# Kernel tuning notes

Hardware: AMD Instinct MI355X
Metric: run time of the kernel (lower is better)

The kernel has to match this reference:

```python
import jax, jax.numpy as jnp
import numpy as np

H = 16  # head_num

def _rope(x, cos, sin):
    # x: [B,H,T,dh]; cos/sin: [T, dh//2]
    xr = x.reshape(*x.shape[:-1], -1, 2)
    re, im = xr[..., 0], xr[..., 1]
    out_re = re * cos - im * sin
    out_im = re * sin + im * cos
    return jnp.stack([out_re, out_im], axis=-1).reshape(x.shape)

def setup_inputs() -> dict:
    key = jax.random.key(0)
    ks = jax.random.split(key, 5)
    B, T, D = 2, 2048, 1024
    s = 1.0 / np.sqrt(D)
    return {
        "embedding_word": jax.random.normal(ks[0], (B, T, D), jnp.float32),
        "wq": jax.random.normal(ks[1], (D, D), jnp.float32) * s,
        "wk": jax.random.normal(ks[2], (D, D), jnp.float32) * s,
        "wv": jax.random.normal(ks[3], (D, D), jnp.float32) * s,
        "wo": jax.random.normal(ks[4], (D, D), jnp.float32) * s,
    }

def reference(embedding_word, wq, wk, wv, wo):
    x = embedding_word
    B, T, D = x.shape
    dh = D // H
    # projections (torch Linear: x @ W.T)
    q = (x @ wq.T).reshape(B, T, H, dh).transpose(0, 2, 1, 3)  # [B,H,T,dh]
    k = (x @ wk.T).reshape(B, T, H, dh).transpose(0, 2, 1, 3)
    v = (x @ wv.T).reshape(B, T, H, dh).transpose(0, 2, 1, 3)
    # rotary embedding (theta=10000)
    freqs = 1.0 / (10000.0 ** (jnp.arange(0, dh, 2, dtype=jnp.float32) / dh))
    ang = jnp.arange(T, dtype=jnp.float32)[:, None] * freqs[None, :]  # [T, dh/2]
    cos, sin = jnp.cos(ang), jnp.sin(ang)
    q = _rope(q, cos, sin)
    k = _rope(k, cos, sin)
    # attention with causal mask; scale after mask as in original
    scores = jnp.einsum("bhqd,bhkd->bhqk", q, k)
    causal = jnp.triu(jnp.ones((T, T), dtype=bool), k=1)
    scores = jnp.where(causal, -jnp.inf, scores)
    weights = jax.nn.softmax(scores / jnp.sqrt(jnp.float32(dh)), axis=-1)
    out = jnp.einsum("bhqk,bhkd->bhqd", weights, v)
    out = out.transpose(0, 2, 1, 3).reshape(B, T, D)
    return out @ wo.T
```

## Files before the change

kernel.cpp:

```cpp
#include <hip/hip_runtime.h>
#include <hip/hip_bf16.h>
#include <math.h>

#define B_  2
#define T_  2048
#define D_  1024
#define H_  16
#define DH_ 64
#define TOK (B_*T_)

typedef __attribute__((ext_vector_type(8))) short bf16x8;
typedef __attribute__((ext_vector_type(4))) float f32x4;

static __device__ __forceinline__ float bf2f(short u) {
    union { unsigned int i; float f; } c;
    c.i = ((unsigned int)(unsigned short)u) << 16;
    return c.f;
}
static __device__ __forceinline__ short f2bf(float f) {
    union { float f; unsigned int i; } c; c.f = f;
    unsigned int r = c.i + 0x7fff + ((c.i >> 16) & 1);
    return (short)(r >> 16);
}

__global__ __launch_bounds__(256) void cast_bf16(const float* __restrict__ in,
                                                 short* __restrict__ out, int n8)
{
    int i = blockIdx.x * 256 + threadIdx.x;
    if (i < n8) {
        const float4* p = reinterpret_cast<const float4*>(in);
        float4 a = p[2*i], b = p[2*i+1];
        bf16x8 o;
        o[0] = f2bf(a.x); o[1] = f2bf(a.y); o[2] = f2bf(a.z); o[3] = f2bf(a.w);
        o[4] = f2bf(b.x); o[5] = f2bf(b.y); o[6] = f2bf(b.z); o[7] = f2bf(b.w);
        reinterpret_cast<bf16x8*>(out)[i] = o;
    }
}

__global__ __launch_bounds__(256) void rope_table(float2* __restrict__ tab)
{
    int idx = blockIdx.x * 256 + threadIdx.x;
    int t = idx >> 5, i = idx & 31;
    float freq = __powf(10000.f, -(float)i * (1.0f / 32.0f));
    float s, c;
    sincosf((float)t * freq, &s, &c);
    tab[idx] = make_float2(c, s);
}

__global__ __launch_bounds__(256) void rope_apply(short* __restrict__ X,
                                                  const float2* __restrict__ tab)
{
    int q = blockIdx.x * 256 + threadIdx.x;
    int p0 = q << 2;
    int tt = (p0 >> 9) & (T_ - 1);
    int i0 = p0 & 31;
    int4 v = reinterpret_cast<int4*>(X)[q];
    int out[4]; int vv[4] = {v.x, v.y, v.z, v.w};
#pragma unroll
    for (int j = 0; j < 4; ++j) {
        float2 cs = tab[tt * 32 + i0 + j];
        float re = bf2f((short)(vv[j] & 0xffff));
        float im = bf2f((short)(((unsigned int)vv[j]) >> 16));
        float nr = re * cs.x - im * cs.y;
        float ni = re * cs.y + im * cs.x;
        out[j] = (int)(unsigned short)f2bf(nr) |
                 ((int)(unsigned short)f2bf(ni) << 16);
    }
    reinterpret_cast<int4*>(X)[q] = make_int4(out[0], out[1], out[2], out[3]);
}

template<int BF16OUT>
__global__ __launch_bounds__(256) void gemm_abt_mfma(
    const short* __restrict__ A,
    const short* __restrict__ B0, const short* __restrict__ B1, const short* __restrict__ B2,
    short* __restrict__ Ob0, short* __restrict__ Ob1, short* __restrict__ Ob2,
    float* __restrict__ Of0, int K)
{
    __shared__ short As[128 * 32];
    __shared__ short Bs[128 * 32];
    const int sel = blockIdx.x >> 3;
    const int bn  = (blockIdx.x & 7) << 7;
    const int bm  = blockIdx.y << 7;
    const short* Bm = sel == 0 ? B0 : (sel == 1 ? B1 : B2);
    short* Obp      = sel == 0 ? Ob0 : (sel == 1 ? Ob1 : Ob2);
    const int tid  = threadIdx.x;
    const int wv   = tid >> 6, lane = tid & 63;
    const int wr   = wv >> 1,  wc   = wv & 1;
    const int fr   = lane & 15, fg  = lane >> 4;
    const int srow  = lane >> 2;
    const int skoff = (lane & 3) << 3;
    f32x4 acc[4][4] = {};

    for (int k0 = 0; k0 < K; k0 += 32) {
        __syncthreads();
#pragma unroll
        for (int it = 0; it < 2; ++it) {
            const int c = wv * 2 + it;
            const int r = 16 * c + srow;
            __builtin_amdgcn_global_load_lds(
                (const __attribute__((address_space(1))) unsigned int*)
                    (A + (size_t)(bm + r) * K + k0 + skoff),
                (__attribute__((address_space(3))) unsigned int*)(As + c * 512),
                16, 0, 0);
            __builtin_amdgcn_global_load_lds(
                (const __attribute__((address_space(1))) unsigned int*)
                    (Bm + (size_t)(bn + r) * K + k0 + skoff),
                (__attribute__((address_space(3))) unsigned int*)(Bs + c * 512),
                16, 0, 0);
        }
        __syncthreads();
        bf16x8 af[4], bfr[4];
#pragma unroll
        for (int m = 0; m < 4; ++m)
            af[m] = *(const bf16x8*)(As + (wr * 64 + m * 16 + fr) * 32 + fg * 8);
#pragma unroll
        for (int n = 0; n < 4; ++n)
            bfr[n] = *(const bf16x8*)(Bs + (wc * 64 + n * 16 + fr) * 32 + fg * 8);
#pragma unroll
        for (int m = 0; m < 4; ++m)
#pragma unroll
            for (int n = 0; n < 4; ++n)
                acc[m][n] = __builtin_amdgcn_mfma_f32_16x16x32_bf16(
                                af[m], bfr[n], acc[m][n], 0, 0, 0);
    }
    const int row0 = bm + wr * 64 + fg * 4;
    const int col0 = bn + wc * 64 + fr;
#pragma unroll
    for (int m = 0; m < 4; ++m)
#pragma unroll
        for (int n = 0; n < 4; ++n)
#pragma unroll
            for (int j = 0; j < 4; ++j) {
                const size_t idx = (size_t)(row0 + m * 16 + j) * 1024 + col0 + n * 16;
                if (BF16OUT) Obp[idx] = f2bf(acc[m][n][j]);
                else         Of0[idx] = acc[m][n][j];
            }
}

__global__ __launch_bounds__(256) void attn_mfma(
    const short* __restrict__ Qb, const short* __restrict__ Kb,
    const short* __restrict__ Vb, short* __restrict__ Ob)
{
    __shared__ short Ks[64 * 64];
    __shared__ short Vt[64 * 64];
    __shared__ short Ps[64 * 64];

    const int qt = (int)(gridDim.x - 1) - (int)blockIdx.x;
    const int bh = blockIdx.y;
    const int b  = bh >> 4, h = bh & 15;
    const int q0 = qt << 6;
    const int tid  = threadIdx.x;
    const int wv   = tid >> 6, lane = tid & 63;
    const int fr   = lane & 15, fg = lane >> 4;

    const size_t qrow = (size_t)(b * T_ + q0 + wv * 16 + fr);
    const short* qp = Qb + qrow * D_ + h * DH_;
    const bf16x8 qf0 = *(const bf16x8*)(qp + fg * 8);
    const bf16x8 qf1 = *(const bf16x8*)(qp + 32 + fg * 8);

    float m_i[4], l_i[4];
    f32x4 oa[4] = {};
#pragma unroll
    for (int j = 0; j < 4; ++j) { m_i[j] = -1e30f; l_i[j] = 0.f; }

    const int sdoff = (tid & 7) << 3;
    const int sr0   = tid >> 3;
    const int sr1   = sr0 + 32;
    const short* kbase = Kb + (size_t)b * T_ * D_ + h * DH_ + sdoff;
    const short* vbase = Vb + (size_t)b * T_ * D_ + h * DH_ + sdoff;

    for (int kt = 0; kt <= qt; ++kt) {
        const int k0 = kt << 6;
        const bf16x8 kr0 = *(const bf16x8*)(kbase + (size_t)(k0 + sr0) * D_);
        const bf16x8 kr1 = *(const bf16x8*)(kbase + (size_t)(k0 + sr1) * D_);
        const bf16x8 vr0 = *(const bf16x8*)(vbase + (size_t)(k0 + sr0) * D_);
        const bf16x8 vr1 = *(const bf16x8*)(vbase + (size_t)(k0 + sr1) * D_);
        __syncthreads();
        *(bf16x8*)(Ks + ((sr0 * 64 + sdoff) ^ ((sr0 & 7) << 3))) = kr0;
        *(bf16x8*)(Ks + ((sr1 * 64 + sdoff) ^ ((sr1 & 7) << 3))) = kr1;
#pragma unroll
        for (int jj = 0; jj < 8; ++jj) {
            const int j0 = (jj + (tid & 7)) & 7;
            const int d0 = sdoff + j0;
            Vt[(d0 * 64 + sr0) ^ ((d0 & 7) << 3)] = vr0[j0];
            Vt[(d0 * 64 + sr1) ^ ((d0 & 7) << 3)] = vr1[j0];
        }
        __syncthreads();

        f32x4 sc[4] = {};
#pragma unroll
        for (int f = 0; f < 4; ++f) {
            const int krow = 16 * f + fr;
            const bf16x8 b0 = *(const bf16x8*)(Ks + ((krow * 64 + fg * 8)      ^ ((krow & 7) << 3)));
            const bf16x8 b1 = *(const bf16x8*)(Ks + ((krow * 64 + 32 + fg * 8) ^ ((krow & 7) << 3)));
            sc[f] = __builtin_amdgcn_mfma_f32_16x16x32_bf16(qf0, b0, sc[f], 0, 0, 0);
            sc[f] = __builtin_amdgcn_mfma_f32_16x16x32_bf16(qf1, b1, sc[f], 0, 0, 0);
        }

#pragma unroll
        for (int j = 0; j < 4; ++j) {
            const int qg = q0 + 16 * wv + 4 * fg + j;
            float pv[4];
#pragma unroll
            for (int f = 0; f < 4; ++f) {
                const int kg = k0 + 16 * f + fr;
                const float x = sc[f][j] * 0.125f;
                pv[f] = (kg <= qg) ? x : -1e30f;
            }
            float mv = fmaxf(fmaxf(pv[0], pv[1]), fmaxf(pv[2], pv[3]));
            mv = fmaxf(mv, __shfl_xor(mv, 1));
            mv = fmaxf(mv, __shfl_xor(mv, 2));
            mv = fmaxf(mv, __shfl_xor(mv, 4));
            mv = fmaxf(mv, __shfl_xor(mv, 8));
            const float mnew = fmaxf(m_i[j], mv);
            const float corr = __expf(m_i[j] - mnew);
            m_i[j] = mnew;
            float ps = 0.f;
            const int qa = 16 * wv + 4 * fg + j;
#pragma unroll
            for (int f = 0; f < 4; ++f) {
                const float e = __expf(pv[f] - mnew);
                ps += e;
                Ps[(qa * 64 + 16 * f + fr) ^ ((qa & 7) << 3)] = f2bf(e);
            }
            ps += __shfl_xor(ps, 1); ps += __shfl_xor(ps, 2);
            ps += __shfl_xor(ps, 4); ps += __shfl_xor(ps, 8);
            l_i[j] = l_i[j] * corr + ps;
#pragma unroll
            for (int n = 0; n < 4; ++n) oa[n][j] *= corr;
        }

#pragma unroll
        for (int kc = 0; kc < 2; ++kc) {
            const int qa = 16 * wv + fr;
            const bf16x8 pa = *(const bf16x8*)(Ps + ((qa * 64 + kc * 32 + fg * 8) ^ ((qa & 7) << 3)));
#pragma unroll
            for (int n = 0; n < 4; ++n) {
                const int dr = 16 * n + fr;
                const bf16x8 vb = *(const bf16x8*)(Vt + ((dr * 64 + kc * 32 + fg * 8) ^ ((dr & 7) << 3)));
                oa[n] = __builtin_amdgcn_mfma_f32_16x16x32_bf16(pa, vb, oa[n], 0, 0, 0);
            }
        }
    }

#pragma unroll
    for (int j = 0; j < 4; ++j) {
        const float inv = 1.f / l_i[j];
        const size_t orow = (size_t)(b * T_ + q0 + 16 * wv + 4 * fg + j);
#pragma unroll
        for (int n = 0; n < 4; ++n)
            Ob[orow * D_ + h * DH_ + 16 * n + fr] = f2bf(oa[n][j] * inv);
    }
}

extern "C" void kernel_launch(void* const* d_in, const int* in_sizes, int n_in,
                              void* d_out, int out_size, void* d_ws, size_t ws_size,
                              hipStream_t stream)
{
    const float* x  = (const float*)d_in[0];
    const float* wq = (const float*)d_in[1];
    const float* wk = (const float*)d_in[2];
    const float* wv = (const float*)d_in[3];
    const float* wo = (const float*)d_in[4];
    float* out = (float*)d_out;

    const size_t NTOK = (size_t)TOK * D_;
    const size_t NW   = (size_t)D_ * D_;
    short* xb  = (short*)d_ws;
    short* wqb = xb  + NTOK;
    short* wkb = wqb + NW;
    short* wvb = wkb + NW;
    short* wob = wvb + NW;
    short* Qb  = wob + NW;
    short* Kb  = Qb  + NTOK;
    short* Vb  = Kb  + NTOK;
    short* Obf = Vb  + NTOK;
    float2* tab = (float2*)(Obf + NTOK);

    cast_bf16<<<2048, 256, 0, stream>>>(x,  xb,  (int)(NTOK / 8));
    cast_bf16<<<512,  256, 0, stream>>>(wq, wqb, (int)(NW / 8));
    cast_bf16<<<512,  256, 0, stream>>>(wk, wkb, (int)(NW / 8));
    cast_bf16<<<512,  256, 0, stream>>>(wv, wvb, (int)(NW / 8));
    cast_bf16<<<512,  256, 0, stream>>>(wo, wob, (int)(NW / 8));
    rope_table<<<256, 256, 0, stream>>>(tab);

    gemm_abt_mfma<1><<<dim3(24, 32), 256, 0, stream>>>(
        xb, wqb, wkb, wvb, Qb, Kb, Vb, nullptr, D_);

    rope_apply<<<2048, 256, 0, stream>>>(Qb, tab);
    rope_apply<<<2048, 256, 0, stream>>>(Kb, tab);

    attn_mfma<<<dim3(T_ / 64, B_ * H_), 256, 0, stream>>>(Qb, Kb, Vb, Obf);

    gemm_abt_mfma<0><<<dim3(8, 32), 256, 0, stream>>>(
        Obf, wob, wob, wob, nullptr, nullptr, nullptr, out, D_);
}
```

Before: 318.1 us.

## Rewrite attention with 32x32 MFMA, register-resident P, double buffering; fuse cast/rope launches

The attention kernel is rewritten so each block handles 128 query rows. It uses 32x32x16 MFMA, keeps the probability tile in registers through lane shuffles instead of shared memory, double-buffers the K/V tiles, and skips the rescale when the running max barely moves. The softmax scale and log2(e) are folded into Q during RoPE, so the kernel can use exp2f. The cast and rope kernels are merged into single launches, and the output is staged through shared memory for coalesced stores. These changes aim to cut LDS traffic, barriers, exp cost and launch overhead, at the price of more registers and bf16 rounding of the pre-scaled Q.

```diff
diff --git a/kernel.cpp b/kernel.cpp
--- a/kernel.cpp
+++ b/kernel.cpp
@@ -9,8 +9,9 @@
 #define DH_ 64
 #define TOK (B_*T_)
 
-typedef __attribute__((ext_vector_type(8))) short bf16x8;
-typedef __attribute__((ext_vector_type(4))) float f32x4;
+typedef __attribute__((ext_vector_type(8)))  short bf16x8;
+typedef __attribute__((ext_vector_type(4)))  float f32x4;
+typedef __attribute__((ext_vector_type(16))) float f32x16;
 
 static __device__ __forceinline__ float bf2f(short u) {
     union { unsigned int i; float f; } c;
@@ -22,19 +23,35 @@
     unsigned int r = c.i + 0x7fff + ((c.i >> 16) & 1);
     return (short)(r >> 16);
 }
-
-__global__ __launch_bounds__(256) void cast_bf16(const float* __restrict__ in,
-                                                 short* __restrict__ out, int n8)
+static __device__ __forceinline__ unsigned cvtpk(float lo, float hi2) {
+    unsigned r;
+    asm("v_cvt_pk_bf16_f32 %0, %1, %2" : "=v"(r) : "v"(lo), "v"(hi2));
+    return r;
+}
+
+__global__ __launch_bounds__(256) void cast_all(
+    const float* __restrict__ x,  const float* __restrict__ wq,
+    const float* __restrict__ wk, const float* __restrict__ wv,
+    const float* __restrict__ wo,
+    short* __restrict__ xb,  short* __restrict__ wqb,
+    short* __restrict__ wkb, short* __restrict__ wvb,
+    short* __restrict__ wob)
 {
     int i = blockIdx.x * 256 + threadIdx.x;
-    if (i < n8) {
-        const float4* p = reinterpret_cast<const float4*>(in);
-        float4 a = p[2*i], b = p[2*i+1];
-        bf16x8 o;
-        o[0] = f2bf(a.x); o[1] = f2bf(a.y); o[2] = f2bf(a.z); o[3] = f2bf(a.w);
-        o[4] = f2bf(b.x); o[5] = f2bf(b.y); o[6] = f2bf(b.z); o[7] = f2bf(b.w);
-        reinterpret_cast<bf16x8*>(out)[i] = o;
-    }
+    const float* src; short* dst; int off;
+    if (i < 524288) { src = x; dst = xb; off = i; }
+    else {
+        int j = i - 524288;
+        int wsel = j >> 17;  off = j & 131071;
+        src = wsel == 0 ? wq : wsel == 1 ? wk : wsel == 2 ? wv : wo;
+        dst = wsel == 0 ? wqb : wsel == 1 ? wkb : wsel == 2 ? wvb : wob;
+    }
+    const float4* p = reinterpret_cast<const float4*>(src);
+    float4 a = p[2*off], b = p[2*off+1];
+    bf16x8 o;
+    o[0] = f2bf(a.x); o[1] = f2bf(a.y); o[2] = f2bf(a.z); o[3] = f2bf(a.w);
+    o[4] = f2bf(b.x); o[5] = f2bf(b.y); o[6] = f2bf(b.z); o[7] = f2bf(b.w);
+    reinterpret_cast<bf16x8*>(dst)[off] = o;
 }
 
 __global__ __launch_bounds__(256) void rope_table(float2* __restrict__ tab)
@@ -47,10 +64,16 @@
     tab[idx] = make_float2(c, s);
 }
 
-__global__ __launch_bounds__(256) void rope_apply(short* __restrict__ X,
-                                                  const float2* __restrict__ tab)
-{
-    int q = blockIdx.x * 256 + threadIdx.x;
+__global__ __launch_bounds__(256) void rope_apply2(short* __restrict__ Q,
+                                                   short* __restrict__ K,
+                                                   const float2* __restrict__ tab)
+{
+    int g = blockIdx.x * 256 + threadIdx.x;
+    short* X;
+    float sc;
+    int q;
+    if (g < 524288) { X = Q; sc = 0.18033688011112042f; q = g; }
+    else            { X = K; sc = 1.0f;                 q = g - 524288; }
     int p0 = q << 2;
     int tt = (p0 >> 9) & (T_ - 1);
     int i0 = p0 & 31;
@@ -61,8 +84,8 @@
         float2 cs = tab[tt * 32 + i0 + j];
         float re = bf2f((short)(vv[j] & 0xffff));
         float im = bf2f((short)(((unsigned int)vv[j]) >> 16));
-        float nr = re * cs.x - im * cs.y;
-        float ni = re * cs.y + im * cs.x;
+        float nr = (re * cs.x - im * cs.y) * sc;
+        float ni = (re * cs.y + im * cs.x) * sc;
         out[j] = (int)(unsigned short)f2bf(nr) |
                  ((int)(unsigned short)f2bf(ni) << 16);
     }
@@ -137,120 +160,167 @@
             }
 }
 
-__global__ __launch_bounds__(256) void attn_mfma(
+__global__ __launch_bounds__(256) void attn_mfma2(
     const short* __restrict__ Qb, const short* __restrict__ Kb,
     const short* __restrict__ Vb, short* __restrict__ Ob)
 {
-    __shared__ short Ks[64 * 64];
-    __shared__ short Vt[64 * 64];
-    __shared__ short Ps[64 * 64];
-
-    const int qt = (int)(gridDim.x - 1) - (int)blockIdx.x;
+    __shared__ short KsBuf[2][64 * 64];
+    __shared__ short VtBuf[2][64 * 64];
+
+    const int qb = (int)(gridDim.x - 1 - blockIdx.x);
     const int bh = blockIdx.y;
     const int b  = bh >> 4, h = bh & 15;
-    const int q0 = qt << 6;
+    const int q0 = qb << 7;
     const int tid  = threadIdx.x;
-    const int wv   = tid >> 6, lane = tid & 63;
-    const int fr   = lane & 15, fg = lane >> 4;
-
-    const size_t qrow = (size_t)(b * T_ + q0 + wv * 16 + fr);
-    const short* qp = Qb + qrow * D_ + h * DH_;
-    const bf16x8 qf0 = *(const bf16x8*)(qp + fg * 8);
-    const bf16x8 qf1 = *(const bf16x8*)(qp + 32 + fg * 8);
-
-    float m_i[4], l_i[4];
-    f32x4 oa[4] = {};
-#pragma unroll
-    for (int j = 0; j < 4; ++j) { m_i[j] = -1e30f; l_i[j] = 0.f; }
-
-    const int sdoff = (tid & 7) << 3;
-    const int sr0   = tid >> 3;
-    const int sr1   = sr0 + 32;
-    const short* kbase = Kb + (size_t)b * T_ * D_ + h * DH_ + sdoff;
-    const short* vbase = Vb + (size_t)b * T_ * D_ + h * DH_ + sdoff;
-
-    for (int kt = 0; kt <= qt; ++kt) {
-        const int k0 = kt << 6;
-        const bf16x8 kr0 = *(const bf16x8*)(kbase + (size_t)(k0 + sr0) * D_);
-        const bf16x8 kr1 = *(const bf16x8*)(kbase + (size_t)(k0 + sr1) * D_);
-        const bf16x8 vr0 = *(const bf16x8*)(vbase + (size_t)(k0 + sr0) * D_);
-        const bf16x8 vr1 = *(const bf16x8*)(vbase + (size_t)(k0 + sr1) * D_);
+    const int w    = tid >> 6, lane = tid & 63;
+    const int ql   = lane & 31, hi = lane >> 5;
+    const int qw_lo  = q0 + 32 * w;
+    const int q_glob = qw_lo + ql;
+    const int nt = (q0 + 128) >> 6;
+
+    const short* qp = Qb + (size_t)(b * T_ + q_glob) * D_ + h * DH_ + hi * 8;
+    bf16x8 qf[4];
+#pragma unroll
+    for (int ds = 0; ds < 4; ++ds)
+        qf[ds] = *(const bf16x8*)(qp + 16 * ds);
+
+    float m_run = -3e38f, l_run = 0.f;
+    f32x16 accO0, accO1;
+#pragma unroll
+    for (int r = 0; r < 16; ++r) { accO0[r] = 0.f; accO1[r] = 0.f; }
+
+    const int sr0 = tid >> 3, sr1 = sr0 + 32, sdo = (tid & 7) << 3;
+    const short* kbase = Kb + (size_t)b * T_ * D_ + h * DH_ + sdo;
+    const short* vbase = Vb + (size_t)b * T_ * D_ + h * DH_ + sdo;
+
+    bf16x8 krA, krB, vrA, vrB;
+#define LOADT(t) {                                                        \
+        const size_t o_ = (size_t)((t) << 6) * D_;                        \
+        krA = *(const bf16x8*)(kbase + o_ + (size_t)sr0 * D_);            \
+        krB = *(const bf16x8*)(kbase + o_ + (size_t)sr1 * D_);            \
+        vrA = *(const bf16x8*)(vbase + o_ + (size_t)sr0 * D_);            \
+        vrB = *(const bf16x8*)(vbase + o_ + (size_t)sr1 * D_); }
+#define STORET(bu) {                                                      \
+        short* Kp = KsBuf[bu]; short* Vp = VtBuf[bu];                     \
+        *(bf16x8*)(Kp + ((sr0 * 64 + sdo) ^ ((sr0 & 7) << 3))) = krA;     \
+        *(bf16x8*)(Kp + ((sr1 * 64 + sdo) ^ ((sr1 & 7) << 3))) = krB;     \
+        _Pragma("unroll")                                                 \
+        for (int jj = 0; jj < 8; ++jj) {                                  \
+            const int j0 = (jj + (tid & 7)) & 7;                          \
+            const int d0 = sdo + j0;                                      \
+            Vp[(d0 * 64 + sr0) ^ ((d0 & 7) << 3)] = vrA[j0];              \
+            Vp[(d0 * 64 + sr1) ^ ((d0 & 7) << 3)] = vrB[j0];              \
+        } }
+
+    LOADT(0); STORET(0);
+    __syncthreads();
+
+    for (int t = 0; t < nt; ++t) {
+        const int cur = t & 1;
+        const int K0  = t << 6;
+        const bool hasNext = (t + 1 < nt);
+        if (hasNext) LOADT(t + 1);
+
+        if (K0 <= qw_lo + 31) {
+            const short* Kp = KsBuf[cur];
+            const short* Vp = VtBuf[cur];
+            f32x16 s0, s1;
+#pragma unroll
+            for (int r = 0; r < 16; ++r) { s0[r] = 0.f; s1[r] = 0.f; }
+#pragma unroll
+            for (int ds = 0; ds < 4; ++ds) {
+                const int c = 16 * ds + 8 * hi;
+                const int r0 = ql, r1 = 32 + ql;
+                bf16x8 kf0 = *(const bf16x8*)(Kp + ((r0 * 64 + c) ^ ((r0 & 7) << 3)));
+                bf16x8 kf1 = *(const bf16x8*)(Kp + ((r1 * 64 + c) ^ ((r1 & 7) << 3)));
+                s0 = __builtin_amdgcn_mfma_f32_32x32x16_bf16(kf0, qf[ds], s0, 0, 0, 0);
+                s1 = __builtin_amdgcn_mfma_f32_32x32x16_bf16(kf1, qf[ds], s1, 0, 0, 0);
+            }
+            if (K0 + 63 > qw_lo) {
+                const int qrel = q_glob - K0;
+#pragma unroll
+                for (int r = 0; r < 16; ++r) {
+                    const int kv0 = 4 * hi + ((r & 3) + 8 * (r >> 2));
+                    s0[r] = (kv0      <= qrel) ? s0[r] : -3e38f;
+                    s1[r] = (kv0 + 32 <= qrel) ? s1[r] : -3e38f;
+                }
+            }
+            float mloc = s0[0];
+#pragma unroll
+            for (int r = 1; r < 16; ++r) mloc = fmaxf(mloc, s0[r]);
+#pragma unroll
+            for (int r = 0; r < 16; ++r) mloc = fmaxf(mloc, s1[r]);
+            mloc = fmaxf(mloc, __shfl_xor(mloc, 32));
+            if (!__all(mloc <= m_run + 11.5f)) {
+                const float mnew = fmaxf(m_run, mloc);
+                const float corr = exp2f(m_run - mnew);
+                m_run = mnew;
+                l_run *= corr;
+#pragma unroll
+                for (int r = 0; r < 16; ++r) { accO0[r] *= corr; accO1[r] *= corr; }
+            }
+            float lsum = 0.f;
+#pragma unroll
+            for (int r = 0; r < 16; ++r) { s0[r] = exp2f(s0[r] - m_run); lsum += s0[r]; }
+#pragma unroll
+            for (int r = 0; r < 16; ++r) { s1[r] = exp2f(s1[r] - m_run); lsum += s1[r]; }
+            lsum += __shfl_xor(lsum, 32);
+            l_run += lsum;
+            unsigned W[8][2];
+#pragma unroll
+            for (int q4 = 0; q4 < 4; ++q4) {
+                W[q4][0]     = cvtpk(s0[4*q4+0], s0[4*q4+1]);
+                W[q4][1]     = cvtpk(s0[4*q4+2], s0[4*q4+3]);
+                W[q4 + 4][0] = cvtpk(s1[4*q4+0], s1[4*q4+1]);
+                W[q4 + 4][1] = cvtpk(s1[4*q4+2], s1[4*q4+3]);
+            }
+#pragma unroll
+            for (int sl = 0; sl < 4; ++sl) {
+                const int qe = 2 * sl, qo = qe + 1;
+                unsigned srcA = hi ? W[qe][0] : W[qo][0];
+                unsigned srcB = hi ? W[qe][1] : W[qo][1];
+                unsigned xA = (unsigned)__shfl_xor((int)srcA, 32);
+                unsigned xB = (unsigned)__shfl_xor((int)srcB, 32);
+                union { unsigned u[4]; bf16x8 v; } pu;
+                pu.u[0] = hi ? xA : W[qe][0];
+                pu.u[1] = hi ? xB : W[qe][1];
+                pu.u[2] = hi ? W[qo][0] : xA;
+                pu.u[3] = hi ? W[qo][1] : xB;
+                const int c = 16 * sl + 8 * hi;
+                const int d0 = ql, d1 = 32 + ql;
+                bf16x8 vf0 = *(const bf16x8*)(Vp + ((d0 * 64 + c) ^ ((d0 & 7) << 3)));
+                bf16x8 vf1 = *(const bf16x8*)(Vp + ((d1 * 64 + c) ^ ((d1 & 7) << 3)));
+                accO0 = __builtin_amdgcn_mfma_f32_32x32x16_bf16(vf0, pu.v, accO0, 0, 0, 0);
+                accO1 = __builtin_amdgcn_mfma_f32_32x32x16_bf16(vf1, pu.v, accO1, 0, 0, 0);
+            }
+        }
+        if (hasNext) STORET(cur ^ 1);
         __syncthreads();
-        *(bf16x8*)(Ks + ((sr0 * 64 + sdoff) ^ ((sr0 & 7) << 3))) = kr0;
-        *(bf16x8*)(Ks + ((sr1 * 64 + sdoff) ^ ((sr1 & 7) << 3))) = kr1;
-#pragma unroll
-        for (int jj = 0; jj < 8; ++jj) {
-            const int j0 = (jj + (tid & 7)) & 7;
-            const int d0 = sdoff + j0;
-            Vt[(d0 * 64 + sr0) ^ ((d0 & 7) << 3)] = vr0[j0];
-            Vt[(d0 * 64 + sr1) ^ ((d0 & 7) << 3)] = vr1[j0];
-        }
-        __syncthreads();
-
-        f32x4 sc[4] = {};
-#pragma unroll
-        for (int f = 0; f < 4; ++f) {
-            const int krow = 16 * f + fr;
-            const bf16x8 b0 = *(const bf16x8*)(Ks + ((krow * 64 + fg * 8)      ^ ((krow & 7) << 3)));
-            const bf16x8 b1 = *(const bf16x8*)(Ks + ((krow * 64 + 32 + fg * 8) ^ ((krow & 7) << 3)));
-            sc[f] = __builtin_amdgcn_mfma_f32_16x16x32_bf16(qf0, b0, sc[f], 0, 0, 0);
-            sc[f] = __builtin_amdgcn_mfma_f32_16x16x32_bf16(qf1, b1, sc[f], 0, 0, 0);
-        }
-
-#pragma unroll
-        for (int j = 0; j < 4; ++j) {
-            const int qg = q0 + 16 * wv + 4 * fg + j;
-            float pv[4];
-#pragma unroll
-            for (int f = 0; f < 4; ++f) {
-                const int kg = k0 + 16 * f + fr;
-                const float x = sc[f][j] * 0.125f;
-                pv[f] = (kg <= qg) ? x : -1e30f;
-            }
-            float mv = fmaxf(fmaxf(pv[0], pv[1]), fmaxf(pv[2], pv[3]));
-            mv = fmaxf(mv, __shfl_xor(mv, 1));
-            mv = fmaxf(mv, __shfl_xor(mv, 2));
-            mv = fmaxf(mv, __shfl_xor(mv, 4));
-            mv = fmaxf(mv, __shfl_xor(mv, 8));
-            const float mnew = fmaxf(m_i[j], mv);
-            const float corr = __expf(m_i[j] - mnew);
-            m_i[j] = mnew;
-            float ps = 0.f;
-            const int qa = 16 * wv + 4 * fg + j;
-#pragma unroll
-            for (int f = 0; f < 4; ++f) {
-                const float e = __expf(pv[f] - mnew);
-                ps += e;
-                Ps[(qa * 64 + 16 * f + fr) ^ ((qa & 7) << 3)] = f2bf(e);
-            }
-            ps += __shfl_xor(ps, 1); ps += __shfl_xor(ps, 2);
-            ps += __shfl_xor(ps, 4); ps += __shfl_xor(ps, 8);
-            l_i[j] = l_i[j] * corr + ps;
-#pragma unroll
-            for (int n = 0; n < 4; ++n) oa[n][j] *= corr;
-        }
-
-#pragma unroll
-        for (int kc = 0; kc < 2; ++kc) {
-            const int qa = 16 * wv + fr;
-            const bf16x8 pa = *(const bf16x8*)(Ps + ((qa * 64 + kc * 32 + fg * 8) ^ ((qa & 7) << 3)));
-#pragma unroll
-            for (int n = 0; n < 4; ++n) {
-                const int dr = 16 * n + fr;
-                const bf16x8 vb = *(const bf16x8*)(Vt + ((dr * 64 + kc * 32 + fg * 8) ^ ((dr & 7) << 3)));
-                oa[n] = __builtin_amdgcn_mfma_f32_16x16x32_bf16(pa, vb, oa[n], 0, 0, 0);
-            }
-        }
-    }
-
-#pragma unroll
-    for (int j = 0; j < 4; ++j) {
-        const float inv = 1.f / l_i[j];
-        const size_t orow = (size_t)(b * T_ + q0 + 16 * wv + 4 * fg + j);
-#pragma unroll
-        for (int n = 0; n < 4; ++n)
-            Ob[orow * D_ + h * DH_ + 16 * n + fr] = f2bf(oa[n][j] * inv);
-    }
+    }
+
+    unsigned* Ot = (unsigned*)KsBuf;
+    const float invl = 1.f / l_run;
+#pragma unroll
+    for (int rq = 0; rq < 4; ++rq) {
+        unsigned p0 = cvtpk(accO0[4*rq+0] * invl, accO0[4*rq+1] * invl);
+        unsigned p1 = cvtpk(accO0[4*rq+2] * invl, accO0[4*rq+3] * invl);
+        unsigned p2 = cvtpk(accO1[4*rq+0] * invl, accO1[4*rq+1] * invl);
+        unsigned p3 = cvtpk(accO1[4*rq+2] * invl, accO1[4*rq+3] * invl);
+        const int du0 = (4 * hi + 8 * rq) >> 1;
+        Ot[w * 1024 + ql * 32 + du0]          = p0;
+        Ot[w * 1024 + ql * 32 + du0 + 1]      = p1;
+        Ot[w * 1024 + ql * 32 + du0 + 16]     = p2;
+        Ot[w * 1024 + ql * 32 + du0 + 16 + 1] = p3;
+    }
+    __syncthreads();
+    {
+        const int qq = tid >> 1, half = tid & 1;
+        const int4* s4 = (const int4*)(Ot + (qq >> 5) * 1024 + (qq & 31) * 32 + half * 16);
+        int4* d4 = (int4*)(Ob + (size_t)(b * T_ + q0 + qq) * D_ + h * DH_ + half * 32);
+        d4[0] = s4[0]; d4[1] = s4[1]; d4[2] = s4[2]; d4[3] = s4[3];
+    }
+#undef LOADT
+#undef STORET
 }
 
 extern "C" void kernel_launch(void* const* d_in, const int* in_sizes, int n_in,
@@ -277,20 +347,16 @@
     short* Obf = Vb  + NTOK;
     float2* tab = (float2*)(Obf + NTOK);
 
-    cast_bf16<<<2048, 256, 0, stream>>>(x,  xb,  (int)(NTOK / 8));
-    cast_bf16<<<512,  256, 0, stream>>>(wq, wqb, (int)(NW / 8));
-    cast_bf16<<<512,  256, 0, stream>>>(wk, wkb, (int)(NW / 8));
-    cast_bf16<<<512,  256, 0, stream>>>(wv, wvb, (int)(NW / 8));
-    cast_bf16<<<512,  256, 0, stream>>>(wo, wob, (int)(NW / 8));
+    cast_all<<<4096, 256, 0, stream>>>(x, wq, wk, wv, wo,
+                                       xb, wqb, wkb, wvb, wob);
     rope_table<<<256, 256, 0, stream>>>(tab);
 
     gemm_abt_mfma<1><<<dim3(24, 32), 256, 0, stream>>>(
         xb, wqb, wkb, wvb, Qb, Kb, Vb, nullptr, D_);
 
-    rope_apply<<<2048, 256, 0, stream>>>(Qb, tab);
-    rope_apply<<<2048, 256, 0, stream>>>(Kb, tab);
-
-    attn_mfma<<<dim3(T_ / 64, B_ * H_), 256, 0, stream>>>(Qb, Kb, Vb, Obf);
+    rope_apply2<<<4096, 256, 0, stream>>>(Qb, Kb, tab);
+
+    attn_mfma2<<<dim3(T_ / 128, B_ * H_), 256, 0, stream>>>(Qb, Kb, Vb, Obf);
 
     gemm_abt_mfma<0><<<dim3(8, 32), 256, 0, stream>>>(
         Obf, wob, wob, wob, nullptr, nullptr, nullptr, out, D_);
```

Result: faster. 276.7 us (-13.0%).
